# Performance work log

Hardware: AMD Instinct MI355X
Metric: run time of the kernel (lower is better)

## Reference

```python
import jax, jax.numpy as jnp
import numpy as np

B, T, C = 4, 2048, 768
N_HEAD = 12
HS = C // N_HEAD

def setup_inputs() -> dict:
    key = jax.random.key(0)
    ks = jax.random.split(key, 5)
    s = 0.02
    return {
        "x": jax.random.normal(ks[0], (B, T, C), dtype=jnp.float32),
        "w_attn": jax.random.normal(ks[1], (C, 3 * C), dtype=jnp.float32) * s,
        "b_attn": jnp.zeros((3 * C,), dtype=jnp.float32),
        "w_proj": jax.random.normal(ks[2], (C, C), dtype=jnp.float32) * s,
        "b_proj": jnp.zeros((C,), dtype=jnp.float32),
    }

def reference(x, w_attn, b_attn, w_proj, b_proj):
    Bx, Tx, Cx = x.shape
    qkv = x @ w_attn + b_attn                      # [B,T,3C]
    q, k, v = jnp.split(qkv, 3, axis=-1)
    # [B,H,T,hs]
    q = q.reshape(Bx, Tx, N_HEAD, HS).transpose(0, 2, 1, 3)
    k = k.reshape(Bx, Tx, N_HEAD, HS).transpose(0, 2, 1, 3)
    v = v.reshape(Bx, Tx, N_HEAD, HS).transpose(0, 2, 1, 3)
    att = jnp.einsum('bhqd,bhkd->bhqk', q, k) * (1.0 / jnp.sqrt(jnp.float32(HS)))
    mask = jnp.tril(jnp.ones((Tx, Tx), dtype=bool))  # causal
    att = jnp.where(mask, att, jnp.float32(-jnp.inf))
    att = jax.nn.softmax(att, axis=-1)
    y = jnp.einsum('bhqk,bhkd->bhqd', att, v)
    y = y.transpose(0, 2, 1, 3).reshape(Bx, Tx, Cx)
    return y @ w_proj + b_proj
```

## Files before the change

### kernel.cpp

```cpp
#include <hip/hip_runtime.h>

#define BB 4
#define TT 2048
#define CC 768
#define QKVW 2304
#define NHH 12
#define HSS 64
#define NQT64 (TT / 64)

typedef __attribute__((ext_vector_type(4))) float floatx4;
typedef __attribute__((ext_vector_type(8))) short shortx8;
typedef __attribute__((ext_vector_type(4))) short shortx4;

__device__ __forceinline__ unsigned short f2bf(float f) {
  union { float f; unsigned int u; } cv; cv.f = f;
  unsigned int u = cv.u;
  u += 0x7FFFu + ((u >> 16) & 1u);
  return (unsigned short)(u >> 16);
}
__device__ __forceinline__ unsigned short bfp(float f) {
  union { float f; unsigned int u; } cv; cv.f = f;
  return (unsigned short)((cv.u + 0x8000u) >> 16);
}
__device__ __forceinline__ unsigned short bft(float f) {
  union { float f; unsigned int u; } cv; cv.f = f;
  return (unsigned short)(cv.u >> 16);
}

__device__ __forceinline__ void async_copy16(const void* g, void* l) {
  __builtin_amdgcn_global_load_lds(
      (const __attribute__((address_space(1))) unsigned int*)g,
      (__attribute__((address_space(3))) unsigned int*)l, 16, 0, 0);
}

__global__ __launch_bounds__(256)
void prep_fused(const float* __restrict__ x, unsigned short* __restrict__ xb, int n4,
                const float* __restrict__ wa, unsigned short* __restrict__ wta,
                const float* __restrict__ wp, unsigned short* __restrict__ wtp) {
  __shared__ short tile[64 * 68];
  const int bid = blockIdx.x;
  const int tid = threadIdx.x;
  if (bid < 1024) {
    int i = bid * 256 + tid;
    const int stride = 1024 * 256;
    for (; i < n4; i += stride) {
      float4 v = ((const float4*)x)[i];
      shortx4 s;
      s.x = (short)f2bf(v.x); s.y = (short)f2bf(v.y);
      s.z = (short)f2bf(v.z); s.w = (short)f2bf(v.w);
      ((shortx4*)xb)[i] = s;
    }
    return;
  }
  const float* w; unsigned short* wt; int N, n0, k0;
  if (bid < 1456) {
    const int t = bid - 1024;
    w = wa; wt = wta; N = QKVW; n0 = (t % 36) * 64; k0 = (t / 36) * 64;
  } else {
    const int t = bid - 1456;
    w = wp; wt = wtp; N = CC;   n0 = (t % 12) * 64; k0 = (t / 12) * 64;
  }
  const int K = CC;
  {
    const int tr = tid >> 4, tc = (tid & 15) * 4;
#pragma unroll
    for (int i = 0; i < 4; ++i) {
      float4 v = *(const float4*)(w + (size_t)(k0 + tr + 16 * i) * N + n0 + tc);
      short* d = &tile[(tr + 16 * i) * 68 + tc];
      d[0] = (short)f2bf(v.x); d[1] = (short)f2bf(v.y);
      d[2] = (short)f2bf(v.z); d[3] = (short)f2bf(v.w);
    }
  }
  __syncthreads();
  {
    const int wr = tid >> 3, wc = (tid & 7) * 8;
#pragma unroll
    for (int j = 0; j < 2; ++j) {
      const int n = wr + 32 * j;
      shortx8 s;
#pragma unroll
      for (int e = 0; e < 8; ++e) s[e] = tile[(wc + e) * 68 + n];
      *(shortx8*)(wt + (size_t)(n0 + n) * K + k0 + wc) = s;
    }
  }
}

__global__ __launch_bounds__(256)
void transpose_v(const unsigned short* __restrict__ qkv, unsigned short* __restrict__ Vt) {
  __shared__ short tile[64 * 72];
  const int t0 = blockIdx.x * 64;
  const int bh = blockIdx.y;
  const int b = bh / NHH, h = bh % NHH;
  const int tid = threadIdx.x;
  {
    const int tr = tid >> 3, tc = (tid & 7) * 8;
#pragma unroll
    for (int i = 0; i < 2; ++i) {
      shortx8 v = *(const shortx8*)(qkv + ((size_t)(b * TT + t0 + tr + 32 * i)) * QKVW + 2 * CC + h * HSS + tc);
      *(shortx8*)&tile[(tr + 32 * i) * 72 + tc] = v;
    }
  }
  __syncthreads();
  {
    const int dr = tid >> 3, tc = (tid & 7) * 8;
    const int base = (tc & 32) + ((tc >> 3) & 3) * 4;
#pragma unroll
    for (int j = 0; j < 2; ++j) {
      const int d = dr + 32 * j;
      shortx8 s;
#pragma unroll
      for (int e = 0; e < 8; ++e)
        s[e] = tile[(base + (e >> 2) * 16 + (e & 3)) * 72 + d];
      *(shortx8*)(Vt + ((size_t)bh * HSS + d) * TT + t0 + tc) = s;
    }
  }
}

template<bool OUT_BF16, bool QSCALE, bool VSTORE>
__global__ __launch_bounds__(256)
void gemm_tn(const unsigned short* __restrict__ A, const unsigned short* __restrict__ Bt,
             const float* __restrict__ bias, void* __restrict__ Cp,
             unsigned short* __restrict__ VtOut, int M, int N, int K) {
  __shared__ short As[3][128 * 32];
  __shared__ short Bs[3][128 * 32];
  const int tid = threadIdx.x, lane = tid & 63, wave = tid >> 6;
  const int row = lane & 15, quad = lane >> 4;
  const int wm = (wave >> 1) * 64, wn = (wave & 1) * 64;
  const int m0 = blockIdx.x * 128, n0 = blockIdx.y * 128;

  floatx4 acc[4][4] = {};

  const int lr = lane >> 2;
  const int csrc = (lane & 3) ^ ((lr >> 1) & 3);
  const int sr = wave * 32 + lr;
  const unsigned short* aP = A + (size_t)(m0 + sr) * K + csrc * 8;
  const unsigned short* bP = Bt + (size_t)(n0 + sr) * K + csrc * 8;
  const int sOff = (wave * 32) * 32;

  const int qsw = (quad ^ ((row >> 1) & 3)) * 8;

  const int nk = K >> 5;

  auto stage = [&](int t, int bi) {
#pragma unroll
    for (int i = 0; i < 2; ++i) {
      async_copy16(aP + (size_t)(16 * i) * K + t * 32, &As[bi][sOff + i * 512]);
      async_copy16(bP + (size_t)(16 * i) * K + t * 32, &Bs[bi][sOff + i * 512]);
    }
  };

  stage(0, 0);
  if (nk > 1) stage(1, 1);
  int cb = 0;
  for (int t = 0; t < nk; ++t) {
    int pb = cb + 2; if (pb >= 3) pb -= 3;
    if (t + 2 < nk) {
      stage(t + 2, pb);
      asm volatile("s_waitcnt vmcnt(8)" ::: "memory");
    } else if (t + 1 < nk) {
      asm volatile("s_waitcnt vmcnt(4)" ::: "memory");
    } else {
      asm volatile("s_waitcnt vmcnt(0)" ::: "memory");
    }
    __builtin_amdgcn_sched_barrier(0);
    __builtin_amdgcn_s_barrier();
    __builtin_amdgcn_sched_barrier(0);
    {
      shortx8 af[4], bf[4];
#pragma unroll
      for (int g = 0; g < 4; ++g) {
        af[g] = *(const shortx8*)&As[cb][(wm + g * 16 + row) * 32 + qsw];
        bf[g] = *(const shortx8*)&Bs[cb][(wn + g * 16 + row) * 32 + qsw];
      }
#pragma unroll
      for (int mg = 0; mg < 4; ++mg)
#pragma unroll
        for (int ng = 0; ng < 4; ++ng)
          acc[mg][ng] = __builtin_amdgcn_mfma_f32_16x16x32_bf16(af[mg], bf[ng], acc[mg][ng], 0, 0, 0);
    }
    __builtin_amdgcn_sched_barrier(0);
    __builtin_amdgcn_s_barrier();
    __builtin_amdgcn_sched_barrier(0);
    cb = (cb + 1 == 3) ? 0 : cb + 1;
  }

  if (VSTORE && n0 >= 2 * CC) {
    const int bb = m0 >> 11;
#pragma unroll
    for (int mg = 0; mg < 4; ++mg) {
      const int tb = (m0 & 2047) + wm + mg * 16 + quad * 4;
      const int t_store = (tb & ~31) | ((tb & 12) << 1) | ((tb >> 2) & 4);
#pragma unroll
      for (int ng = 0; ng < 4; ++ng) {
        const int n = n0 + wn + ng * 16 + row;
        const float bv = bias[n];
        const int f = n - 2 * CC;
        shortx4 pk;
#pragma unroll
        for (int r = 0; r < 4; ++r) pk[r] = (short)f2bf(acc[mg][ng][r] + bv);
        *(shortx4*)(VtOut + ((size_t)(bb * NHH + (f >> 6)) * HSS + (f & 63)) * TT + t_store) = pk;
      }
    }
    return;
  }

#pragma unroll
  for (int mg = 0; mg < 4; ++mg) {
    const int m = m0 + wm + mg * 16 + quad * 4;
#pragma unroll
    for (int ng = 0; ng < 4; ++ng) {
      const int n = n0 + wn + ng * 16 + row;
      const float bv = bias[n];
      const float scl = (QSCALE && n < CC) ? 0.180336881f : 1.0f;
#pragma unroll
      for (int r = 0; r < 4; ++r) {
        const float val = (acc[mg][ng][r] + bv) * scl;
        if (OUT_BF16) ((unsigned short*)Cp)[(size_t)(m + r) * N + n] = f2bf(val);
        else          ((float*)Cp)[(size_t)(m + r) * N + n] = val;
      }
    }
  }
}

__global__ __launch_bounds__(256)
void attn_kernel(const unsigned short* __restrict__ qkv, const unsigned short* __restrict__ Vt,
                 unsigned short* __restrict__ y) {
  __shared__ short Ksh[3][64 * 64];
  __shared__ short Vsh[3][64 * 64];

  const int id = blockIdx.x;
  const int xcd = id & 7;
  const int slot = id >> 3;
  const int qt = NQT64 - 1 - slot / 6;
  const int gl = slot % 6;
  const int g = xcd * 6 + gl;
  const int h = g % NHH, b = g / NHH;
  const int bh = b * NHH + h;
  const int tid = threadIdx.x, lane = tid & 63, wave = tid >> 6;
  const int row = lane & 15, quad = lane >> 4;
  const int qhalf = wave & 1;
  const int khalf = wave >> 1;

  const unsigned short* kSrc = qkv + ((size_t)(b * TT)) * QKVW + CC + h * HSS;
  const unsigned short* vSrc = Vt + ((size_t)bh * HSS) * TT;

  const shortx8 ones8 = {(short)0x3F80, (short)0x3F80, (short)0x3F80, (short)0x3F80,
                         (short)0x3F80, (short)0x3F80, (short)0x3F80, (short)0x3F80};

  const int qb0 = qt * 64 + qhalf * 32;
  const int nk = qt + 1;

  const int lr8 = lane >> 3;
  const int csw = ((lane & 7) ^ lr8) * 8;
  size_t kOff[2], vOff[2];
#pragma unroll
  for (int i = 0; i < 2; ++i) {
    const int r = wave * 16 + i * 8 + lr8;
    kOff[i] = (size_t)r * QKVW + csw;
    vOff[i] = (size_t)r * TT + csw;
  }
  const int sBase = (wave * 16) * 64;

  const int r7 = row & 7;
  int kR[2][2], vR[4];
#pragma unroll
  for (int mg = 0; mg < 2; ++mg) {
    const int krow = khalf * 32 + mg * 16 + row;
    kR[mg][0] = krow * 64 + ((quad ^ r7) * 8);
    kR[mg][1] = krow * 64 + (((quad + 4) ^ r7) * 8);
  }
#pragma unroll
  for (int dg = 0; dg < 4; ++dg)
    vR[dg] = (dg * 16 + row) * 64 + (((khalf * 4 + quad) ^ r7) * 8);

  shortx8 qf[2][2];
#pragma unroll
  for (int qg = 0; qg < 2; ++qg) {
    const unsigned short* qp = qkv + ((size_t)(b * TT) + qb0 + qg * 16 + row) * QKVW + h * HSS;
    qf[qg][0] = *(const shortx8*)(qp + quad * 8);
    qf[qg][1] = *(const shortx8*)(qp + 32 + quad * 8);
  }
  asm volatile("s_waitcnt vmcnt(0)" ::: "memory");

  floatx4 lf[2] = {(floatx4)(0.0f), (floatx4)(0.0f)};
  floatx4 o[2][4];
#pragma unroll
  for (int qg = 0; qg < 2; ++qg)
#pragma unroll
    for (int dg = 0; dg < 4; ++dg) o[qg][dg] = (floatx4)(0.0f);

  auto stage = [&](int t, int bi) {
#pragma unroll
    for (int i = 0; i < 2; ++i) {
      async_copy16(kSrc + (size_t)(t * 64) * QKVW + kOff[i], &Ksh[bi][sBase + i * 512]);
      async_copy16(vSrc + (size_t)(t * 64) + vOff[i],        &Vsh[bi][sBase + i * 512]);
    }
  };

  stage(0, 0);
  if (nk > 1) stage(1, 1);
  int cb = 0;
  for (int kt = 0; kt < nk; ++kt) {
    int pb = cb + 2; if (pb >= 3) pb -= 3;
    if (kt + 2 < nk) {
      stage(kt + 2, pb);
      asm volatile("s_waitcnt vmcnt(8)" ::: "memory");
    } else if (kt + 1 < nk) {
      asm volatile("s_waitcnt vmcnt(4)" ::: "memory");
    } else {
      asm volatile("s_waitcnt vmcnt(0)" ::: "memory");
    }
    __builtin_amdgcn_sched_barrier(0);
    __builtin_amdgcn_s_barrier();
    __builtin_amdgcn_sched_barrier(0);
    {
      const short* Kc = &Ksh[cb][0];
      const short* Vc = &Vsh[cb][0];
      __builtin_amdgcn_s_setprio(1);
      shortx4 pfr[2][2];
#pragma unroll
      for (int mg = 0; mg < 2; ++mg) {
        const shortx8 kf0 = *(const shortx8*)&Kc[kR[mg][0]];
        const shortx8 kf1 = *(const shortx8*)&Kc[kR[mg][1]];
#pragma unroll
        for (int qg = 0; qg < 2; ++qg) {
          floatx4 t = __builtin_amdgcn_mfma_f32_16x16x32_bf16(kf0, qf[qg][0], (floatx4)(0.0f), 0, 0, 0);
          t = __builtin_amdgcn_mfma_f32_16x16x32_bf16(kf1, qf[qg][1], t, 0, 0, 0);
          if (kt == qt) {
            const int kg = kt * 64 + khalf * 32 + mg * 16 + quad * 4;
            const int qv = qb0 + qg * 16 + row;
#pragma unroll
            for (int r = 0; r < 4; ++r)
              if (kg + r > qv) t[r] = -1e30f;
          }
          shortx4 pk;
#pragma unroll
          for (int r = 0; r < 4; ++r) pk[r] = (short)bft(__builtin_amdgcn_exp2f(t[r]));
          pfr[qg][mg] = pk;
        }
      }
      shortx8 pk8[2];
#pragma unroll
      for (int qg = 0; qg < 2; ++qg) {
        pk8[qg] = __builtin_shufflevector(pfr[qg][0], pfr[qg][1], 0, 1, 2, 3, 4, 5, 6, 7);
        lf[qg] = __builtin_amdgcn_mfma_f32_16x16x32_bf16(pk8[qg], ones8, lf[qg], 0, 0, 0);
      }
#pragma unroll
      for (int dg = 0; dg < 4; ++dg) {
        const shortx8 vf = *(const shortx8*)&Vc[vR[dg]];
#pragma unroll
        for (int qg = 0; qg < 2; ++qg)
          o[qg][dg] = __builtin_amdgcn_mfma_f32_16x16x32_bf16(pk8[qg], vf, o[qg][dg], 0, 0, 0);
      }
      __builtin_amdgcn_s_setprio(0);
    }
    __builtin_amdgcn_sched_barrier(0);
    __builtin_amdgcn_s_barrier();
    __builtin_amdgcn_sched_barrier(0);
    cb = (cb + 1 == 3) ? 0 : cb + 1;
  }

  floatx4* red4 = (floatx4*)(&Ksh[0][0]);
  const int rbase = (qhalf * 64 + lane) * 11;
  if (khalf) {
#pragma unroll
    for (int qg = 0; qg < 2; ++qg) {
#pragma unroll
      for (int dg = 0; dg < 4; ++dg) red4[rbase + qg * 4 + dg] = o[qg][dg];
      red4[rbase + 8 + qg] = lf[qg];
    }
  }
  __syncthreads();
  if (!khalf) {
#pragma unroll
    for (int qg = 0; qg < 2; ++qg) {
#pragma unroll
      for (int dg = 0; dg < 4; ++dg) o[qg][dg] += red4[rbase + qg * 4 + dg];
      lf[qg] += red4[rbase + 8 + qg];
    }
#pragma unroll
    for (int qg = 0; qg < 2; ++qg) {
#pragma unroll
      for (int r = 0; r < 4; ++r) {
        const float lo = 1.0f / lf[qg][r];
        unsigned short* yp = y + ((size_t)(b * TT) + qb0 + qg * 16 + quad * 4 + r) * CC + h * HSS;
#pragma unroll
        for (int dg = 0; dg < 4; ++dg)
          yp[dg * 16 + row] = bfp(o[qg][dg][r] * lo);
      }
    }
  }
}

extern "C" void kernel_launch(void* const* d_in, const int* in_sizes, int n_in,
                              void* d_out, int out_size, void* d_ws, size_t ws_size,
                              hipStream_t stream) {
  const float* x      = (const float*)d_in[0];
  const float* w_attn = (const float*)d_in[1];
  const float* b_attn = (const float*)d_in[2];
  const float* w_proj = (const float*)d_in[3];
  const float* b_proj = (const float*)d_in[4];
  float* out = (float*)d_out;

  char* ws = (char*)d_ws;
  const int M = BB * TT;
  const size_t vtBytes = (size_t)BB * NHH * HSS * TT * 2;

  unsigned short* xb  = (unsigned short*)ws;
  unsigned short* y   = (unsigned short*)ws;
  unsigned short* qkv = (unsigned short*)(ws + 12582912);
  unsigned short* wta = (unsigned short*)(ws + 50331648);

  const bool fusedV = ws_size >= (size_t)53870592 + vtBytes + 1179648;
  unsigned short* Vt  = (unsigned short*)(ws + (fusedV ? (size_t)53870592 : (size_t)50331648));
  unsigned short* wtp = (unsigned short*)(ws + (fusedV ? (size_t)53870592 + vtBytes
                                                       : (size_t)62914560));

  prep_fused<<<1600, 256, 0, stream>>>(x, xb, (M * CC) / 4, w_attn, wta, w_proj, wtp);

  if (fusedV) {
    gemm_tn<true, true, true><<<dim3(M / 128, QKVW / 128), 256, 0, stream>>>(
        xb, wta, b_attn, (void*)qkv, Vt, M, QKVW, CC);
  } else {
    gemm_tn<true, true, false><<<dim3(M / 128, QKVW / 128), 256, 0, stream>>>(
        xb, wta, b_attn, (void*)qkv, nullptr, M, QKVW, CC);
    transpose_v<<<dim3(TT / 64, BB * NHH), 256, 0, stream>>>(qkv, Vt);
  }

  attn_kernel<<<dim3(NQT64 * NHH * BB), 256, 0, stream>>>(qkv, Vt, y);

  gemm_tn<false, false, false><<<dim3(M / 128, CC / 128), 256, 0, stream>>>(
      y, wtp, b_proj, (void*)out, nullptr, M, CC, CC);
}
```

Baseline: 203.6 us.

## Use 256x128 tile QKV GEMM and drop fused V-transpose epilogue

Adds a dedicated QKV projection GEMM with 256x128 block tiles, so each wave computes a 128x64 sub-tile with 32 accumulators, giving more reuse of each B-fragment load. It removes the fused path that wrote V transposed straight from the GEMM epilogue and always runs the separate transpose_v kernel. The larger tile raises register and LDS use, which lowers occupancy and halves the grid along M. The separate transpose adds an extra kernel launch and an extra read and write of V.

```diff
diff --git a/kernel.cpp b/kernel.cpp
--- a/kernel.cpp
+++ b/kernel.cpp
@@ -116,11 +116,94 @@
   }
 }
 
-template<bool OUT_BF16, bool QSCALE, bool VSTORE>
+__global__ __launch_bounds__(256)
+void gemm1_256(const unsigned short* __restrict__ A, const unsigned short* __restrict__ Bt,
+               const float* __restrict__ bias, unsigned short* __restrict__ C,
+               int M, int N, int K) {
+  __shared__ short As[3][256 * 32];
+  __shared__ short Bs[3][128 * 32];
+  const int tid = threadIdx.x, lane = tid & 63, wave = tid >> 6;
+  const int row = lane & 15, quad = lane >> 4;
+  const int wm = (wave >> 1) * 128, wn = (wave & 1) * 64;
+  const int m0 = blockIdx.x * 256, n0 = blockIdx.y * 128;
+
+  floatx4 acc[8][4] = {};
+
+  const int lr = lane >> 2;
+  const int csrc = (lane & 3) ^ ((lr >> 1) & 3);
+  const unsigned short* aP = A + (size_t)(m0 + wave * 64 + lr) * K + csrc * 8;
+  const unsigned short* bP = Bt + (size_t)(n0 + wave * 32 + lr) * K + csrc * 8;
+  const int aOff = (wave * 64) * 32;
+  const int bOff = (wave * 32) * 32;
+
+  const int qsw = (quad ^ ((row >> 1) & 3)) * 8;
+
+  const int nk = K >> 5;
+
+  auto stage = [&](int t, int bi) {
+#pragma unroll
+    for (int i = 0; i < 4; ++i)
+      async_copy16(aP + (size_t)(16 * i) * K + t * 32, &As[bi][aOff + i * 512]);
+#pragma unroll
+    for (int i = 0; i < 2; ++i)
+      async_copy16(bP + (size_t)(16 * i) * K + t * 32, &Bs[bi][bOff + i * 512]);
+  };
+
+  stage(0, 0);
+  stage(1, 1);
+  int cb = 0;
+  for (int t = 0; t < nk; ++t) {
+    int pb = cb + 2; if (pb >= 3) pb -= 3;
+    if (t + 2 < nk) {
+      stage(t + 2, pb);
+      asm volatile("s_waitcnt vmcnt(12)" ::: "memory");
+    } else if (t + 1 < nk) {
+      asm volatile("s_waitcnt vmcnt(6)" ::: "memory");
+    } else {
+      asm volatile("s_waitcnt vmcnt(0)" ::: "memory");
+    }
+    __builtin_amdgcn_sched_barrier(0);
+    __builtin_amdgcn_s_barrier();
+    __builtin_amdgcn_sched_barrier(0);
+    {
+      shortx8 af[8], bf[4];
+#pragma unroll
+      for (int g = 0; g < 8; ++g)
+        af[g] = *(const shortx8*)&As[cb][(wm + g * 16 + row) * 32 + qsw];
+#pragma unroll
+      for (int g = 0; g < 4; ++g)
+        bf[g] = *(const shortx8*)&Bs[cb][(wn + g * 16 + row) * 32 + qsw];
+#pragma unroll
+      for (int mg = 0; mg < 8; ++mg)
+#pragma unroll
+        for (int ng = 0; ng < 4; ++ng)
+          acc[mg][ng] = __builtin_amdgcn_mfma_f32_16x16x32_bf16(af[mg], bf[ng], acc[mg][ng], 0, 0, 0);
+    }
+    __builtin_amdgcn_sched_barrier(0);
+    __builtin_amdgcn_s_barrier();
+    __builtin_amdgcn_sched_barrier(0);
+    cb = (cb + 1 == 3) ? 0 : cb + 1;
+  }
+
+#pragma unroll
+  for (int mg = 0; mg < 8; ++mg) {
+    const int m = m0 + wm + mg * 16 + quad * 4;
+#pragma unroll
+    for (int ng = 0; ng < 4; ++ng) {
+      const int n = n0 + wn + ng * 16 + row;
+      const float bv = bias[n];
+      const float scl = (n < CC) ? 0.180336881f : 1.0f;
+#pragma unroll
+      for (int r = 0; r < 4; ++r)
+        C[(size_t)(m + r) * N + n] = f2bf((acc[mg][ng][r] + bv) * scl);
+    }
+  }
+}
+
+template<bool OUT_BF16, bool QSCALE>
 __global__ __launch_bounds__(256)
 void gemm_tn(const unsigned short* __restrict__ A, const unsigned short* __restrict__ Bt,
-             const float* __restrict__ bias, void* __restrict__ Cp,
-             unsigned short* __restrict__ VtOut, int M, int N, int K) {
+             const float* __restrict__ bias, void* __restrict__ Cp, int M, int N, int K) {
   __shared__ short As[3][128 * 32];
   __shared__ short Bs[3][128 * 32];
   const int tid = threadIdx.x, lane = tid & 63, wave = tid >> 6;
@@ -184,26 +267,6 @@
     cb = (cb + 1 == 3) ? 0 : cb + 1;
   }
 
-  if (VSTORE && n0 >= 2 * CC) {
-    const int bb = m0 >> 11;
-#pragma unroll
-    for (int mg = 0; mg < 4; ++mg) {
-      const int tb = (m0 & 2047) + wm + mg * 16 + quad * 4;
-      const int t_store = (tb & ~31) | ((tb & 12) << 1) | ((tb >> 2) & 4);
-#pragma unroll
-      for (int ng = 0; ng < 4; ++ng) {
-        const int n = n0 + wn + ng * 16 + row;
-        const float bv = bias[n];
-        const int f = n - 2 * CC;
-        shortx4 pk;
-#pragma unroll
-        for (int r = 0; r < 4; ++r) pk[r] = (short)f2bf(acc[mg][ng][r] + bv);
-        *(shortx4*)(VtOut + ((size_t)(bb * NHH + (f >> 6)) * HSS + (f & 63)) * TT + t_store) = pk;
-      }
-    }
-    return;
-  }
-
 #pragma unroll
   for (int mg = 0; mg < 4; ++mg) {
     const int m = m0 + wm + mg * 16 + quad * 4;
@@ -403,32 +466,24 @@
   float* out = (float*)d_out;
 
   char* ws = (char*)d_ws;
-  const int M = BB * TT;
-  const size_t vtBytes = (size_t)BB * NHH * HSS * TT * 2;
-
   unsigned short* xb  = (unsigned short*)ws;
   unsigned short* y   = (unsigned short*)ws;
   unsigned short* qkv = (unsigned short*)(ws + 12582912);
   unsigned short* wta = (unsigned short*)(ws + 50331648);
-
-  const bool fusedV = ws_size >= (size_t)53870592 + vtBytes + 1179648;
-  unsigned short* Vt  = (unsigned short*)(ws + (fusedV ? (size_t)53870592 : (size_t)50331648));
-  unsigned short* wtp = (unsigned short*)(ws + (fusedV ? (size_t)53870592 + vtBytes
-                                                       : (size_t)62914560));
+  unsigned short* Vt  = (unsigned short*)(ws + 50331648);
+  unsigned short* wtp = (unsigned short*)(ws + 62914560);
+
+  const int M = BB * TT;
 
   prep_fused<<<1600, 256, 0, stream>>>(x, xb, (M * CC) / 4, w_attn, wta, w_proj, wtp);
 
-  if (fusedV) {
-    gemm_tn<true, true, true><<<dim3(M / 128, QKVW / 128), 256, 0, stream>>>(
-        xb, wta, b_attn, (void*)qkv, Vt, M, QKVW, CC);
-  } else {
-    gemm_tn<true, true, false><<<dim3(M / 128, QKVW / 128), 256, 0, stream>>>(
-        xb, wta, b_attn, (void*)qkv, nullptr, M, QKVW, CC);
-    transpose_v<<<dim3(TT / 64, BB * NHH), 256, 0, stream>>>(qkv, Vt);
-  }
+  gemm1_256<<<dim3(M / 256, QKVW / 128), 256, 0, stream>>>(
+      xb, wta, b_attn, qkv, M, QKVW, CC);
+
+  transpose_v<<<dim3(TT / 64, BB * NHH), 256, 0, stream>>>(qkv, Vt);
 
   attn_kernel<<<dim3(NQT64 * NHH * BB), 256, 0, stream>>>(qkv, Vt, y);
 
-  gemm_tn<false, false, false><<<dim3(M / 128, CC / 128), 256, 0, stream>>>(
-      y, wtp, b_proj, (void*)out, nullptr, M, CC, CC);
-}
+  gemm_tn<false, false><<<dim3(M / 128, CC / 128), 256, 0, stream>>>(
+      y, wtp, b_proj, (void*)out, M, CC, CC);
+}
```

After: 231.4 us. +13.6%, slower.
